# Kernel optimization log

Measured on AMD Instinct MI355X. Metric: run time of the kernel, lower is better.

Reference implementation:

```python
import jax, jax.numpy as jnp
import numpy as np

N_NODES = 100000
N_EDGES = 1600000
IN_CH = 128
OUT_CH = 32
HID = 2 * OUT_CH


def setup_inputs() -> dict:
    key = jax.random.key(0)
    k1, k2, k3, k4 = jax.random.split(key, 4)
    x = jax.random.normal(k1, (N_NODES, IN_CH), dtype=jnp.float32)
    edge_index = jax.random.randint(k2, (2, N_EDGES), 0, N_NODES, dtype=jnp.int64)
    W1 = jax.random.normal(k3, (IN_CH, HID), dtype=jnp.float32) / np.sqrt(IN_CH)
    b1 = jnp.zeros((HID,), dtype=jnp.float32)
    W2 = jax.random.normal(k4, (HID, OUT_CH), dtype=jnp.float32) / np.sqrt(HID)
    b2 = jnp.zeros((OUT_CH,), dtype=jnp.float32)
    return {"x": x, "edge_index": edge_index, "W1": W1, "b1": b1, "W2": W2, "b2": b2}


def _gcn_norm(edge_index, n_nodes):
    # GCNConv default: add self-loops, symmetric deg^{-1/2} normalization.
    loop = jnp.arange(n_nodes, dtype=edge_index.dtype)
    src = jnp.concatenate([edge_index[0], loop])
    dst = jnp.concatenate([edge_index[1], loop])
    deg = jax.ops.segment_sum(jnp.ones_like(dst, dtype=jnp.float32), dst, num_segments=n_nodes)
    dinv = jnp.where(deg > 0, jax.lax.rsqrt(deg), 0.0)
    norm = dinv[src] * dinv[dst]  # [E + N]
    return src, dst, norm


def _gcn_conv(h, W, b, src, dst, norm, n_nodes):
    m = h @ W                      # transform first (small GEMM)
    msg = m[src] * norm[:, None]   # gather + scale per edge
    agg = jax.ops.segment_sum(msg, dst, num_segments=n_nodes)  # scatter-add
    return agg + b


def reference(x, edge_index, W1, b1, W2, b2):
    n = x.shape[0]
    src, dst, norm = _gcn_norm(edge_index, n)
    h = jax.nn.relu(_gcn_conv(x, W1, b1, src, dst, norm, n))
    return _gcn_conv(h, W2, b2, src, dst, norm, n)
```

## Files before the change

kernel.cpp:

```cpp
#include <hip/hip_runtime.h>

#define IN_CH 128
#define HID 64
#define OUT_CH 32
#define BUCKET_CAP 6144
#define NB_MAX 512

__device__ __forceinline__ unsigned short f32_to_bf16(float f) {
    union { float f; unsigned int u; } v; v.f = f;
    unsigned int u = v.u;
    u += 0x7FFFu + ((u >> 16) & 1u);
    return (unsigned short)(u >> 16);
}
__device__ __forceinline__ float bf16_to_f32(unsigned short h) {
    union { unsigned int u; float f; } v; v.u = ((unsigned int)h) << 16;
    return v.f;
}
__device__ __forceinline__ float bf16_lo(unsigned int u) {
    union { unsigned int u; float f; } v; v.u = u << 16; return v.f;
}
__device__ __forceinline__ float bf16_hi(unsigned int u) {
    union { unsigned int u; float f; } v; v.u = u & 0xFFFF0000u; return v.f;
}

__device__ __forceinline__ int load_idx(const void* e, long long i, int is64) {
    if (is64) return ((const int*)e)[2 * i];
    return ((const int*)e)[i];
}

__global__ __launch_bounds__(256) void binA_kernel(
    const void* __restrict__ edges, long long E,
    int* __restrict__ bucket_cur, unsigned int* __restrict__ entries, int nb) {
    __shared__ int hist[NB_MAX];
    __shared__ int cbase[NB_MAX];
    __shared__ int s_is64;
    const int tid = threadIdx.x;

    if (tid < 64) {
        int v = ((const int*)edges)[2 * tid + 1];
        unsigned long long nz = __ballot(v != 0);
        if (tid == 0) s_is64 = (nz == 0ull) ? 1 : 0;
    }
    for (int i = tid; i < nb; i += 256) hist[i] = 0;
    __syncthreads();
    const int is64 = s_is64;

    const long long per = (E + gridDim.x - 1) / gridDim.x;
    const long long lo = blockIdx.x * per;
    const long long hi = (lo + per < E) ? lo + per : E;

    for (long long i = lo + tid; i < hi; i += 256) {
        int dst = load_idx(edges, E + i, is64);
        atomicAdd(&hist[dst >> 8], 1);
    }
    __syncthreads();
    for (int i = tid; i < nb; i += 256) {
        int c = hist[i];
        int base = (c > 0) ? atomicAdd(&bucket_cur[i], c) : 0;
        cbase[i] = base;
        hist[i] = 0;
    }
    __syncthreads();
    for (long long i = lo + tid; i < hi; i += 256) {
        int src = load_idx(edges, i, is64);
        int dst = load_idx(edges, E + i, is64);
        int b = dst >> 8;
        int rel = cbase[b] + atomicAdd(&hist[b], 1);
        if (rel < BUCKET_CAP)
            entries[(long long)b * BUCKET_CAP + rel] = ((unsigned)src << 8) | (unsigned)(dst & 255);
    }
}

__global__ __launch_bounds__(256) void binB1_kernel(
    const unsigned int* __restrict__ entries, const int* __restrict__ bucket_cur,
    int* __restrict__ counts, int* __restrict__ row_off, float* __restrict__ dinv,
    int n) {
    __shared__ int hist[256];
    __shared__ int scan[256];
    const int b   = blockIdx.x;
    const int tid = threadIdx.x;
    const long long seg = (long long)b * BUCKET_CAP;
    int cnt = bucket_cur[b];
    if (cnt > BUCKET_CAP) cnt = BUCKET_CAP;

    hist[tid] = 0;
    __syncthreads();
    for (int i = tid; i < cnt; i += 256)
        atomicAdd(&hist[entries[seg + i] & 255], 1);
    __syncthreads();

    int v = hist[tid];
    scan[tid] = v;
    __syncthreads();
    for (int off = 1; off < 256; off <<= 1) {
        int t = (tid >= off) ? scan[tid - off] : 0;
        __syncthreads();
        scan[tid] += t;
        __syncthreads();
    }
    int ex = scan[tid] - v;
    int node = (b << 8) + tid;
    if (node < n) {
        counts[node]  = v;
        row_off[node] = (int)seg + ex;
        dinv[node]    = rsqrtf((float)v + 1.0f);
    }
}

__global__ __launch_bounds__(256) void binB2_kernel(
    const unsigned int* __restrict__ entries, const int* __restrict__ bucket_cur,
    const int* __restrict__ row_off, const float* __restrict__ dinv,
    int2* __restrict__ ew, int n) {
    __shared__ int cur[256];
    __shared__ float ldi[256];
    const int b   = blockIdx.x;
    const int tid = threadIdx.x;
    const long long seg = (long long)b * BUCKET_CAP;
    int cnt = bucket_cur[b];
    if (cnt > BUCKET_CAP) cnt = BUCKET_CAP;

    int node = (b << 8) + tid;
    cur[tid] = (node < n) ? row_off[node] - (int)seg : 0;
    ldi[tid] = (node < n) ? dinv[node] : 0.f;
    __syncthreads();

    for (int i = tid; i < cnt; i += 256) {
        unsigned e = entries[seg + i];
        int d = (int)(e & 255u);
        int s = (int)(e >> 8);
        int r = atomicAdd(&cur[d], 1);
        float w = dinv[s] * ldi[d];
        int2 o; o.x = s; o.y = __float_as_int(w);
        ew[seg + r] = o;
    }
}

#define PADX 68
__global__ __launch_bounds__(256) void gemm1_kernel(
    const float* __restrict__ x, const float* __restrict__ W1,
    unsigned short* __restrict__ m1bf, int n) {
    __shared__ __align__(16) float sW[IN_CH * HID];
    __shared__ __align__(16) float sX[64 * PADX];
    const int tid = threadIdx.x;

    {
        const float4* Wv = (const float4*)W1;
        float4* sWv = (float4*)sW;
        for (int i = tid; i < IN_CH * HID / 4; i += 256) sWv[i] = Wv[i];
    }

    const int R0 = blockIdx.x * 64;
    const int tx = tid & 15;
    const int ty = tid >> 4;
    float acc[4][4] = {};

    for (int kt = 0; kt < 2; ++kt) {
        __syncthreads();
        for (int i = tid; i < 64 * 16; i += 256) {
            int r = i >> 4;
            int k4 = i & 15;
            int row = R0 + r;
            float4 v = make_float4(0.f, 0.f, 0.f, 0.f);
            if (row < n)
                v = ((const float4*)(x + (long long)row * IN_CH))[kt * 16 + k4];
            sX[(k4 * 4 + 0) * PADX + r] = v.x;
            sX[(k4 * 4 + 1) * PADX + r] = v.y;
            sX[(k4 * 4 + 2) * PADX + r] = v.z;
            sX[(k4 * 4 + 3) * PADX + r] = v.w;
        }
        __syncthreads();

        const float* pX = sX + ty * 4;
        const float* pW = sW + (kt * 64) * HID + tx * 4;
#pragma unroll 8
        for (int k = 0; k < 64; ++k) {
            float4 xv = *(const float4*)(pX + k * PADX);
            float4 wv = *(const float4*)(pW + k * HID);
            acc[0][0] += xv.x * wv.x; acc[0][1] += xv.x * wv.y;
            acc[0][2] += xv.x * wv.z; acc[0][3] += xv.x * wv.w;
            acc[1][0] += xv.y * wv.x; acc[1][1] += xv.y * wv.y;
            acc[1][2] += xv.y * wv.z; acc[1][3] += xv.y * wv.w;
            acc[2][0] += xv.z * wv.x; acc[2][1] += xv.z * wv.y;
            acc[2][2] += xv.z * wv.z; acc[2][3] += xv.z * wv.w;
            acc[3][0] += xv.w * wv.x; acc[3][1] += xv.w * wv.y;
            acc[3][2] += xv.w * wv.z; acc[3][3] += xv.w * wv.w;
        }
    }

#pragma unroll
    for (int i = 0; i < 4; ++i) {
        int row = R0 + ty * 4 + i;
        if (row < n) {
            ushort4 o;
            o.x = f32_to_bf16(acc[i][0]);
            o.y = f32_to_bf16(acc[i][1]);
            o.z = f32_to_bf16(acc[i][2]);
            o.w = f32_to_bf16(acc[i][3]);
            *(ushort4*)(m1bf + (long long)row * HID + tx * 4) = o;
        }
    }
}

#define PADH 132
__global__ __launch_bounds__(256) void gemm2_kernel(
    const unsigned short* __restrict__ hbf, const float* __restrict__ W2,
    unsigned short* __restrict__ m2bf, int n) {
    __shared__ __align__(16) float sW[HID * OUT_CH];
    __shared__ __align__(16) float sH[HID * PADH];
    const int tid = threadIdx.x;

    {
        const float4* Wv = (const float4*)W2;
        float4* sWv = (float4*)sW;
        for (int i = tid; i < HID * OUT_CH / 4; i += 256) sWv[i] = Wv[i];
    }

    const int R0 = blockIdx.x * 128;
    for (int i = tid; i < 128 * 8; i += 256) {
        int r = i >> 3;
        int q = i & 7;
        int row = R0 + r;
        uint4 v = make_uint4(0u, 0u, 0u, 0u);
        if (row < n)
            v = ((const uint4*)(hbf + (long long)row * HID))[q];
        int k0 = q * 8;
        sH[(k0 + 0) * PADH + r] = bf16_lo(v.x);
        sH[(k0 + 1) * PADH + r] = bf16_hi(v.x);
        sH[(k0 + 2) * PADH + r] = bf16_lo(v.y);
        sH[(k0 + 3) * PADH + r] = bf16_hi(v.y);
        sH[(k0 + 4) * PADH + r] = bf16_lo(v.z);
        sH[(k0 + 5) * PADH + r] = bf16_hi(v.z);
        sH[(k0 + 6) * PADH + r] = bf16_lo(v.w);
        sH[(k0 + 7) * PADH + r] = bf16_hi(v.w);
    }
    __syncthreads();

    const int tx = tid & 7;
    const int ty = tid >> 3;
    float acc[4][4] = {};
    const float* pH = sH + ty * 4;
    const float* pW = sW + tx * 4;
#pragma unroll 8
    for (int k = 0; k < HID; ++k) {
        float4 hv = *(const float4*)(pH + k * PADH);
        float4 wv = *(const float4*)(pW + k * OUT_CH);
        acc[0][0] += hv.x * wv.x; acc[0][1] += hv.x * wv.y;
        acc[0][2] += hv.x * wv.z; acc[0][3] += hv.x * wv.w;
        acc[1][0] += hv.y * wv.x; acc[1][1] += hv.y * wv.y;
        acc[1][2] += hv.y * wv.z; acc[1][3] += hv.y * wv.w;
        acc[2][0] += hv.z * wv.x; acc[2][1] += hv.z * wv.y;
        acc[2][2] += hv.z * wv.z; acc[2][3] += hv.z * wv.w;
        acc[3][0] += hv.w * wv.x; acc[3][1] += hv.w * wv.y;
        acc[3][2] += hv.w * wv.z; acc[3][3] += hv.w * wv.w;
    }

#pragma unroll
    for (int i = 0; i < 4; ++i) {
        int row = R0 + ty * 4 + i;
        if (row < n) {
            ushort4 o;
            o.x = f32_to_bf16(acc[i][0]);
            o.y = f32_to_bf16(acc[i][1]);
            o.z = f32_to_bf16(acc[i][2]);
            o.w = f32_to_bf16(acc[i][3]);
            *(ushort4*)(m2bf + (long long)row * OUT_CH + tx * 4) = o;
        }
    }
}

__global__ __launch_bounds__(256) void gather64_kernel(
    const int* __restrict__ row_off, const int* __restrict__ counts,
    const int2* __restrict__ ew, const float* __restrict__ dinv,
    const unsigned short* __restrict__ m1bf, const float* __restrict__ b1,
    unsigned short* __restrict__ hbf, int n) {
    int node = blockIdx.x * 4 + (threadIdx.x >> 6);
    int lane = threadIdx.x & 63;
    if (node >= n) return;
    int start = __builtin_amdgcn_readfirstlane(row_off[node]);
    int cnt   = __builtin_amdgcn_readfirstlane(counts[node]);
    float dd  = dinv[node];
    float acc = bf16_to_f32(m1bf[(unsigned)(node * HID) + lane]) * dd * dd + b1[lane];
    int j = 0;
    for (; j + 15 < cnt; j += 16) {
        int2 e[16];
#pragma unroll
        for (int u = 0; u < 16; ++u) e[u] = ew[start + j + u];
        float v[16];
#pragma unroll
        for (int u = 0; u < 16; ++u)
            v[u] = bf16_to_f32(m1bf[(unsigned)(e[u].x * HID) + lane]);
#pragma unroll
        for (int u = 0; u < 16; ++u) acc += v[u] * __int_as_float(e[u].y);
    }
    for (; j + 7 < cnt; j += 8) {
        int2 e[8];
#pragma unroll
        for (int u = 0; u < 8; ++u) e[u] = ew[start + j + u];
        float v[8];
#pragma unroll
        for (int u = 0; u < 8; ++u)
            v[u] = bf16_to_f32(m1bf[(unsigned)(e[u].x * HID) + lane]);
#pragma unroll
        for (int u = 0; u < 8; ++u) acc += v[u] * __int_as_float(e[u].y);
    }
    for (; j + 3 < cnt; j += 4) {
        int2 e[4];
#pragma unroll
        for (int u = 0; u < 4; ++u) e[u] = ew[start + j + u];
        float v[4];
#pragma unroll
        for (int u = 0; u < 4; ++u)
            v[u] = bf16_to_f32(m1bf[(unsigned)(e[u].x * HID) + lane]);
#pragma unroll
        for (int u = 0; u < 4; ++u) acc += v[u] * __int_as_float(e[u].y);
    }
    for (; j < cnt; ++j) {
        int2 e = ew[start + j];
        acc += bf16_to_f32(m1bf[(unsigned)(e.x * HID) + lane]) * __int_as_float(e.y);
    }
    hbf[(unsigned)(node * HID) + lane] = f32_to_bf16(fmaxf(acc, 0.f));
}

__global__ __launch_bounds__(256) void gather32_kernel(
    const int* __restrict__ row_off, const int* __restrict__ counts,
    const int2* __restrict__ ew, const float* __restrict__ dinv,
    const unsigned short* __restrict__ m2bf, const float* __restrict__ b2,
    float* __restrict__ out, int n) {
    int node = blockIdx.x * 4 + (threadIdx.x >> 6);
    int lane = threadIdx.x & 63;
    int c    = lane & 31;
    int p    = lane >> 5;
    if (node >= n) return;
    int start = __builtin_amdgcn_readfirstlane(row_off[node]);
    int cnt   = __builtin_amdgcn_readfirstlane(counts[node]);
    float dd  = dinv[node];
    float acc = 0.f;
    int j = 0;
    for (; j + 15 < cnt; j += 16) {
        int2 e[16];
#pragma unroll
        for (int u = 0; u < 16; ++u) e[u] = ew[start + j + u];
#pragma unroll
        for (int u = 0; u < 8; ++u) {
            int2 ea = e[2 * u];
            int2 eb = e[2 * u + 1];
            int   sx = p ? eb.x : ea.x;
            float wv = __int_as_float(p ? eb.y : ea.y);
            acc += bf16_to_f32(m2bf[(unsigned)(sx * OUT_CH) + c]) * wv;
        }
    }
    for (; j + 7 < cnt; j += 8) {
        int2 e[8];
#pragma unroll
        for (int u = 0; u < 8; ++u) e[u] = ew[start + j + u];
#pragma unroll
        for (int u = 0; u < 4; ++u) {
            int2 ea = e[2 * u];
            int2 eb = e[2 * u + 1];
            int   sx = p ? eb.x : ea.x;
            float wv = __int_as_float(p ? eb.y : ea.y);
            acc += bf16_to_f32(m2bf[(unsigned)(sx * OUT_CH) + c]) * wv;
        }
    }
    for (; j + 3 < cnt; j += 4) {
        int2 e[4];
#pragma unroll
        for (int u = 0; u < 4; ++u) e[u] = ew[start + j + u];
#pragma unroll
        for (int u = 0; u < 2; ++u) {
            int2 ea = e[2 * u];
            int2 eb = e[2 * u + 1];
            int   sx = p ? eb.x : ea.x;
            float wv = __int_as_float(p ? eb.y : ea.y);
            acc += bf16_to_f32(m2bf[(unsigned)(sx * OUT_CH) + c]) * wv;
        }
    }
    for (; j < cnt; j += 2) {
        int q = j + p;
        int2 e = ew[start + ((q < cnt) ? q : j)];
        float w = (q < cnt) ? __int_as_float(e.y) : 0.f;
        acc += bf16_to_f32(m2bf[(unsigned)(e.x * OUT_CH) + c]) * w;
    }
    acc += __shfl_xor(acc, 32, 64);
    if (p == 0) {
        float self = bf16_to_f32(m2bf[(unsigned)(node * OUT_CH) + c]);
        out[(unsigned)(node * OUT_CH) + c] = acc + self * dd * dd + b2[c];
    }
}

extern "C" void kernel_launch(void* const* d_in, const int* in_sizes, int n_in,
                              void* d_out, int out_size, void* d_ws, size_t ws_size,
                              hipStream_t stream) {
    const float* x     = (const float*)d_in[0];
    const void*  edges = d_in[1];
    const float* W1    = (const float*)d_in[2];
    const float* b1    = (const float*)d_in[3];
    const float* W2    = (const float*)d_in[4];
    const float* b2    = (const float*)d_in[5];
    float* out = (float*)d_out;

    const int n = in_sizes[0] / IN_CH;
    const long long E = (long long)in_sizes[1] / 2;
    const int nb = (n + 255) / 256;

    float* ws         = (float*)d_ws;
    float* dinv       = ws;
    unsigned short* m1bf = (unsigned short*)(ws + n);
    unsigned short* m2bf = m1bf;
    float* agg        = ws + n + (long long)n * HID / 2;
    unsigned int* entries = (unsigned int*)agg;
    unsigned short* hbf   = (unsigned short*)agg;
    int*   counts     = (int*)(agg + (long long)n * HID);
    int*   row_off    = counts + n;
    int*   bucket_cur = row_off + n;
    int2*  ew         = (int2*)(bucket_cur + NB_MAX);

    hipMemsetAsync(bucket_cur, 0, NB_MAX * sizeof(int), stream);

    binA_kernel<<<256, 256, 0, stream>>>(edges, E, bucket_cur, entries, nb);
    binB1_kernel<<<nb, 256, 0, stream>>>(entries, bucket_cur, counts, row_off, dinv, n);
    binB2_kernel<<<nb, 256, 0, stream>>>(entries, bucket_cur, row_off, dinv, ew, n);

    gemm1_kernel<<<(n + 63) / 64, 256, 0, stream>>>(x, W1, m1bf, n);
    gather64_kernel<<<(n + 3) / 4, 256, 0, stream>>>(
        row_off, counts, ew, dinv, m1bf, b1, hbf, n);

    gemm2_kernel<<<(n + 127) / 128, 256, 0, stream>>>(hbf, W2, m2bf, n);
    gather32_kernel<<<(n + 3) / 4, 256, 0, stream>>>(
        row_off, counts, ew, dinv, m2bf, b2, out, n);
}
```

Before: 265.6 us.

## Run first GEMM on MFMA with split-bf16 three-product emulation of fp32

Replaces the scalar FMA fp32 GEMM for x@W1 with MFMA bf16 instructions. Each fp32 operand is split into bf16 hi and lo parts, and three MFMA products are summed to approximate fp32 accuracy. A small prep kernel splits and transposes W1 into global memory, and B fragments are read directly from global memory rather than staged in LDS. This cuts ALU work and the large LDS W tile. The cost is an extra launch, the hi/lo conversion work on x, and narrower scattered 2-byte output stores.

```diff
diff --git a/kernel.cpp b/kernel.cpp
--- a/kernel.cpp
+++ b/kernel.cpp
@@ -6,6 +6,9 @@
 #define BUCKET_CAP 6144
 #define NB_MAX 512
 
+typedef __attribute__((ext_vector_type(8))) short bf16x8;
+typedef __attribute__((ext_vector_type(4))) float f32x4;
+
 __device__ __forceinline__ unsigned short f32_to_bf16(float f) {
     union { float f; unsigned int u; } v; v.f = f;
     unsigned int u = v.u;
@@ -21,6 +24,9 @@
 }
 __device__ __forceinline__ float bf16_hi(unsigned int u) {
     union { unsigned int u; float f; } v; v.u = u & 0xFFFF0000u; return v.f;
+}
+__device__ __forceinline__ unsigned int pack2(unsigned short a, unsigned short b) {
+    return (unsigned)a | ((unsigned)b << 16);
 }
 
 __device__ __forceinline__ int load_idx(const void* e, long long i, int is64) {
@@ -135,68 +141,80 @@
     }
 }
 
-#define PADX 68
+__global__ __launch_bounds__(256) void prep_w1_kernel(
+    const float* __restrict__ W1,
+    unsigned short* __restrict__ Wt_hi, unsigned short* __restrict__ Wt_lo) {
+    int i = blockIdx.x * 256 + threadIdx.x;
+    if (i >= IN_CH * HID) return;
+    int k = i >> 6, nn = i & 63;
+    float w = W1[i];
+    unsigned short hi = f32_to_bf16(w);
+    unsigned short lo = f32_to_bf16(w - bf16_to_f32(hi));
+    Wt_hi[nn * IN_CH + k] = hi;
+    Wt_lo[nn * IN_CH + k] = lo;
+}
+
+#define XPAD 136
 __global__ __launch_bounds__(256) void gemm1_kernel(
-    const float* __restrict__ x, const float* __restrict__ W1,
-    unsigned short* __restrict__ m1bf, int n) {
-    __shared__ __align__(16) float sW[IN_CH * HID];
-    __shared__ __align__(16) float sX[64 * PADX];
+    const float* __restrict__ x, const unsigned short* __restrict__ Wt_hi,
+    const unsigned short* __restrict__ Wt_lo, unsigned short* __restrict__ m1bf,
+    int n) {
+    __shared__ __align__(16) unsigned short sXhi[64 * XPAD];
+    __shared__ __align__(16) unsigned short sXlo[64 * XPAD];
     const int tid = threadIdx.x;
-
-    {
-        const float4* Wv = (const float4*)W1;
-        float4* sWv = (float4*)sW;
-        for (int i = tid; i < IN_CH * HID / 4; i += 256) sWv[i] = Wv[i];
-    }
-
     const int R0 = blockIdx.x * 64;
-    const int tx = tid & 15;
-    const int ty = tid >> 4;
-    float acc[4][4] = {};
-
-    for (int kt = 0; kt < 2; ++kt) {
-        __syncthreads();
-        for (int i = tid; i < 64 * 16; i += 256) {
-            int r = i >> 4;
-            int k4 = i & 15;
-            int row = R0 + r;
-            float4 v = make_float4(0.f, 0.f, 0.f, 0.f);
+
+#pragma unroll
+    for (int it = 0; it < 8; ++it) {
+        int idx = tid + it * 256;
+        int r = idx >> 5, c4 = idx & 31;
+        int row = R0 + r;
+        float4 v = make_float4(0.f, 0.f, 0.f, 0.f);
+        if (row < n) v = ((const float4*)(x + (long long)row * IN_CH))[c4];
+        unsigned short h0 = f32_to_bf16(v.x), h1 = f32_to_bf16(v.y);
+        unsigned short h2 = f32_to_bf16(v.z), h3 = f32_to_bf16(v.w);
+        unsigned short l0 = f32_to_bf16(v.x - bf16_to_f32(h0));
+        unsigned short l1 = f32_to_bf16(v.y - bf16_to_f32(h1));
+        unsigned short l2 = f32_to_bf16(v.z - bf16_to_f32(h2));
+        unsigned short l3 = f32_to_bf16(v.w - bf16_to_f32(h3));
+        *(uint2*)&sXhi[r * XPAD + c4 * 4] = make_uint2(pack2(h0, h1), pack2(h2, h3));
+        *(uint2*)&sXlo[r * XPAD + c4 * 4] = make_uint2(pack2(l0, l1), pack2(l2, l3));
+    }
+    __syncthreads();
+
+    const int w  = tid >> 6;
+    const int lane = tid & 63;
+    const int ln = lane & 15;
+    const int q  = lane >> 4;
+
+    f32x4 acc[4];
+#pragma unroll
+    for (int nt = 0; nt < 4; ++nt) acc[nt] = (f32x4){0.f, 0.f, 0.f, 0.f};
+
+    const int arow = w * 16 + ln;
+#pragma unroll
+    for (int kc = 0; kc < 4; ++kc) {
+        int aoff = arow * XPAD + kc * 32 + q * 8;
+        bf16x8 a_hi = *(const bf16x8*)&sXhi[aoff];
+        bf16x8 a_lo = *(const bf16x8*)&sXlo[aoff];
+#pragma unroll
+        for (int nt = 0; nt < 4; ++nt) {
+            int boff = (nt * 16 + ln) * IN_CH + kc * 32 + q * 8;
+            bf16x8 b_hi = *(const bf16x8*)&Wt_hi[boff];
+            bf16x8 b_lo = *(const bf16x8*)&Wt_lo[boff];
+            acc[nt] = __builtin_amdgcn_mfma_f32_16x16x32_bf16(a_hi, b_hi, acc[nt], 0, 0, 0);
+            acc[nt] = __builtin_amdgcn_mfma_f32_16x16x32_bf16(a_lo, b_hi, acc[nt], 0, 0, 0);
+            acc[nt] = __builtin_amdgcn_mfma_f32_16x16x32_bf16(a_hi, b_lo, acc[nt], 0, 0, 0);
+        }
+    }
+
+#pragma unroll
+    for (int nt = 0; nt < 4; ++nt) {
+#pragma unroll
+        for (int r = 0; r < 4; ++r) {
+            int row = R0 + w * 16 + q * 4 + r;
             if (row < n)
-                v = ((const float4*)(x + (long long)row * IN_CH))[kt * 16 + k4];
-            sX[(k4 * 4 + 0) * PADX + r] = v.x;
-            sX[(k4 * 4 + 1) * PADX + r] = v.y;
-            sX[(k4 * 4 + 2) * PADX + r] = v.z;
-            sX[(k4 * 4 + 3) * PADX + r] = v.w;
-        }
-        __syncthreads();
-
-        const float* pX = sX + ty * 4;
-        const float* pW = sW + (kt * 64) * HID + tx * 4;
-#pragma unroll 8
-        for (int k = 0; k < 64; ++k) {
-            float4 xv = *(const float4*)(pX + k * PADX);
-            float4 wv = *(const float4*)(pW + k * HID);
-            acc[0][0] += xv.x * wv.x; acc[0][1] += xv.x * wv.y;
-            acc[0][2] += xv.x * wv.z; acc[0][3] += xv.x * wv.w;
-            acc[1][0] += xv.y * wv.x; acc[1][1] += xv.y * wv.y;
-            acc[1][2] += xv.y * wv.z; acc[1][3] += xv.y * wv.w;
-            acc[2][0] += xv.z * wv.x; acc[2][1] += xv.z * wv.y;
-            acc[2][2] += xv.z * wv.z; acc[2][3] += xv.z * wv.w;
-            acc[3][0] += xv.w * wv.x; acc[3][1] += xv.w * wv.y;
-            acc[3][2] += xv.w * wv.z; acc[3][3] += xv.w * wv.w;
-        }
-    }
-
-#pragma unroll
-    for (int i = 0; i < 4; ++i) {
-        int row = R0 + ty * 4 + i;
-        if (row < n) {
-            ushort4 o;
-            o.x = f32_to_bf16(acc[i][0]);
-            o.y = f32_to_bf16(acc[i][1]);
-            o.z = f32_to_bf16(acc[i][2]);
-            o.w = f32_to_bf16(acc[i][3]);
-            *(ushort4*)(m1bf + (long long)row * HID + tx * 4) = o;
+                m1bf[(long long)row * HID + nt * 16 + ln] = f32_to_bf16(acc[nt][r]);
         }
     }
 }
@@ -414,14 +432,17 @@
     int*   row_off    = counts + n;
     int*   bucket_cur = row_off + n;
     int2*  ew         = (int2*)(bucket_cur + NB_MAX);
+    unsigned short* Wt_hi = (unsigned short*)(ew + (long long)nb * BUCKET_CAP);
+    unsigned short* Wt_lo = Wt_hi + IN_CH * HID;
 
     hipMemsetAsync(bucket_cur, 0, NB_MAX * sizeof(int), stream);
 
+    prep_w1_kernel<<<(IN_CH * HID + 255) / 256, 256, 0, stream>>>(W1, Wt_hi, Wt_lo);
     binA_kernel<<<256, 256, 0, stream>>>(edges, E, bucket_cur, entries, nb);
     binB1_kernel<<<nb, 256, 0, stream>>>(entries, bucket_cur, counts, row_off, dinv, n);
     binB2_kernel<<<nb, 256, 0, stream>>>(entries, bucket_cur, row_off, dinv, ew, n);
 
-    gemm1_kernel<<<(n + 63) / 64, 256, 0, stream>>>(x, W1, m1bf, n);
+    gemm1_kernel<<<(n + 63) / 64, 256, 0, stream>>>(x, Wt_hi, Wt_lo, m1bf, n);
     gather64_kernel<<<(n + 3) / 4, 256, 0, stream>>>(
         row_off, counts, ew, dinv, m1bf, b1, hbf, n);
 
```

Result: slower. 278.6 us (+4.9%).
